# Performance work log

Hardware: AMD Instinct MI355X
Metric: run time of the kernel (lower is better)

## Reference

```python
import jax, jax.numpy as jnp
import numpy as np

E = 256   # hidden_dim
H = 2     # num_heads
DH = E // H
EPS = 1e-5


def setup_inputs() -> dict:
    key = jax.random.key(0)
    ks = jax.random.split(key, 20)
    L, S, MAXLOOP = 8192, 8192, 16
    rel = jax.random.randint(ks[0], (L, MAXLOOP), 0, S)
    # sprinkle some padding sentinels (-1 / -2) like real edge loops
    pad = jax.random.uniform(ks[1], (L, MAXLOOP)) < 0.25
    rel = jnp.where(pad, -1, rel)
    rel = rel.at[:, 0].set(jnp.abs(rel[:, 0]) % S)  # ensure >=1 valid edge per face
    inp = {
        'v_face_edge_loop': rel.astype(jnp.int64) if jax.config.jax_enable_x64 else rel.astype(jnp.int32),
        'v_face_mask': jnp.ones((L,), dtype=bool),
        'v_edge_embedding': jax.random.normal(ks[2], (S, E), jnp.float32),
        'v_face_embedding': jax.random.normal(ks[3], (L, E), jnp.float32),
    }
    def w(k, shape):
        return (jax.random.normal(k, shape, jnp.float32) * 0.02)
    for i, base in ((1, 4), (2, 10)):
        inp[f'w_in{i}'] = w(ks[base + 0], (3 * E, E))
        inp[f'b_in{i}'] = jnp.zeros((3 * E,), jnp.float32)
        inp[f'w_out{i}'] = w(ks[base + 1], (E, E))
        inp[f'b_out{i}'] = jnp.zeros((E,), jnp.float32)
        inp[f'ln{i}_g'] = jnp.ones((E,), jnp.float32)
        inp[f'ln{i}_b'] = jnp.zeros((E,), jnp.float32)
    return inp


def _build_mask(face_edge_loop, S):
    # True = disallowed (torch bool attn_mask semantics).
    L = face_edge_loop.shape[0]
    rel = face_edge_loop
    invalid = (rel == -1) | (rel == -2)
    rel = jnp.where(invalid, S, rel)  # scatter invalids into sentinel column S
    mask = jnp.ones((L, S + 1), dtype=bool)
    mask = mask.at[jnp.arange(L)[:, None], rel].set(False)
    return mask[:, :S]  # [L, S]


def _mha(x, kv, mask, w_in, b_in, w_out, b_out):
    # torch nn.MultiheadAttention (unbatched, eval/no-dropout)
    wq, wk, wv = jnp.split(w_in, 3, axis=0)
    bq, bk, bv = jnp.split(b_in, 3, axis=0)
    L, S = x.shape[0], kv.shape[0]
    q = (x @ wq.T + bq).reshape(L, H, DH)
    k = (kv @ wk.T + bk).reshape(S, H, DH)
    v = (kv @ wv.T + bv).reshape(S, H, DH)
    scores = jnp.einsum('lhd,shd->hls', q, k) / np.sqrt(DH).astype(np.float32)
    scores = jnp.where(mask[None, :, :], jnp.float32(-1e9), scores)
    attn = jax.nn.softmax(scores, axis=-1)          # [H, L, S]
    out = jnp.einsum('hls,shd->lhd', attn, v).reshape(L, E)
    return out @ w_out.T + b_out


def _layernorm(x, g, b):
    m = x.mean(-1, keepdims=True)
    var = ((x - m) ** 2).mean(-1, keepdims=True)
    return (x - m) / jnp.sqrt(var + EPS) * g + b


def reference(v_face_edge_loop, v_face_mask, v_edge_embedding, v_face_embedding,
              w_in1, b_in1, w_out1, b_out1, ln1_g, ln1_b,
              w_in2, b_in2, w_out2, b_out2, ln2_g, ln2_b):
    S = v_edge_embedding.shape[0]
    # v_face_mask is all-True here (static shapes); loop[mask] == loop
    mask = _build_mask(v_face_edge_loop, S)
    x = v_face_embedding
    x = x + _mha(x, v_edge_embedding, mask, w_in1, b_in1, w_out1, b_out1)
    x = _layernorm(x, ln1_g, ln1_b)
    x = x + _mha(x, v_edge_embedding, mask, w_in2, b_in2, w_out2, b_out2)
    x = _layernorm(x, ln2_g, ln2_b)
    return x
```

## Files before the change

kernel.cpp:

```cpp
#include <hip/hip_runtime.h>
#include <hip/hip_bf16.h>

typedef short short8 __attribute__((ext_vector_type(8)));
typedef short short4v __attribute__((ext_vector_type(4)));
typedef float f32x4 __attribute__((ext_vector_type(4)));

#define E 256
#define DH 128

__device__ __forceinline__ float bf2f(__hip_bfloat16 x) { return __bfloat162float(x); }
__device__ __forceinline__ __hip_bfloat16 f2bf(float x) { return __float2bfloat16(x); }

struct CvtArgs { const float* in[6]; __hip_bfloat16* out[6]; int n[6]; };

__global__ __launch_bounds__(256) void f2b_all(CvtArgs a)
{
    int seg = blockIdx.y;
    int i = (blockIdx.x * 256 + threadIdx.x) * 8;
    if (i >= a.n[seg]) return;
    const float* in = a.in[seg];
    float4 x = *reinterpret_cast<const float4*>(in + i);
    float4 y = *reinterpret_cast<const float4*>(in + i + 4);
    __hip_bfloat16* o = a.out[seg] + i;
    o[0] = f2bf(x.x); o[1] = f2bf(x.y); o[2] = f2bf(x.z); o[3] = f2bf(x.w);
    o[4] = f2bf(y.x); o[5] = f2bf(y.y); o[6] = f2bf(y.z); o[7] = f2bf(y.w);
}

struct ProjSeg { const __hip_bfloat16* A; const __hip_bfloat16* W; const float* b; __hip_bfloat16* out; };
struct ProjArgs { ProjSeg seg[5]; };

__global__ __launch_bounds__(256) void gemm_proj(ProjArgs args, int M)
{
    int wv = threadIdx.x >> 6, lane = threadIdx.x & 63;
    int m0 = blockIdx.x * 32;
    if (m0 >= M) return;
    ProjSeg sg = args.seg[blockIdx.y];
    int lo = lane & 15, hi = lane >> 4;

    const __hip_bfloat16* arow0 = sg.A + (size_t)(m0 + lo) * E + hi * 8;
    const __hip_bfloat16* arow1 = arow0 + 16 * E;
    const __hip_bfloat16* brow  = sg.W + (size_t)(wv * 64 + lo) * E + hi * 8;

    f32x4 acc[2][4] = {};
#pragma unroll
    for (int k = 0; k < 8; ++k) {
        short8 a0 = *reinterpret_cast<const short8*>(arow0 + k * 32);
        short8 a1 = *reinterpret_cast<const short8*>(arow1 + k * 32);
#pragma unroll
        for (int nt = 0; nt < 4; ++nt) {
            short8 b = *reinterpret_cast<const short8*>(brow + (size_t)nt * 16 * E + k * 32);
            acc[0][nt] = __builtin_amdgcn_mfma_f32_16x16x32_bf16(a0, b, acc[0][nt], 0, 0, 0);
            acc[1][nt] = __builtin_amdgcn_mfma_f32_16x16x32_bf16(a1, b, acc[1][nt], 0, 0, 0);
        }
    }
#pragma unroll
    for (int nt = 0; nt < 4; ++nt) {
        int col = wv * 64 + nt * 16 + lo;
        float bias = sg.b[col];
#pragma unroll
        for (int mt = 0; mt < 2; ++mt)
#pragma unroll
            for (int r = 0; r < 4; ++r) {
                int row = m0 + mt * 16 + hi * 4 + r;
                sg.out[(size_t)row * E + col] = f2bf(acc[mt][nt][r] + bias);
            }
    }
}

__global__ __launch_bounds__(256) void attn_outproj_ln(
    const int* __restrict__ rel, const __hip_bfloat16* __restrict__ q16,
    const __hip_bfloat16* __restrict__ k16, const __hip_bfloat16* __restrict__ v16,
    const __hip_bfloat16* __restrict__ wout, const float* __restrict__ bout,
    const float* __restrict__ resid, const float* __restrict__ lng, const float* __restrict__ lnb,
    float* __restrict__ xres_out, __hip_bfloat16* __restrict__ xbf_out,
    float* __restrict__ final_out, int L, int ML)
{
    __shared__ __align__(16) __hip_bfloat16 atile[16 * 264];
    __shared__ float sm[16 * 260];
    __shared__ float red[256], red2[256];
    __shared__ float mv[16], rs[16];
    __shared__ __align__(16) float lds_w[4][2][16];
    __shared__ int lds_idx[4][16];

    int tid = threadIdx.x, wv = tid >> 6, lane = tid & 63;
    int m0 = blockIdx.x * 16;
    int g = lane >> 2, q = lane & 3;
    const float scale = 0.088388347648318447f;

    for (int it = 0; it < 4; ++it) {
        int r = wv * 4 + it;
        int face = m0 + r;
        const int* rr = rel + (size_t)face * ML;
        int myidx = (g < ML) ? rr[g] : -1;

        bool dup = false;
#pragma unroll
        for (int d = 1; d < 16; ++d) {
            int other = __shfl(myidx, ((g - d) & 15) * 4 + q);
            if (d <= g && other == myidx) dup = true;
        }
        bool myuse = (myidx >= 0) && !dup;
        int safe = myidx < 0 ? 0 : myidx;
        if (q == 0) lds_idx[wv][g] = safe;

        short8 qv[2][4];
#pragma unroll
        for (int h = 0; h < 2; ++h)
#pragma unroll
            for (int t = 0; t < 4; ++t)
                qv[h][t] = *reinterpret_cast<const short8*>(
                    q16 + (size_t)face * E + h * DH + (t * 4 + q) * 8);

#pragma unroll
        for (int h = 0; h < 2; ++h) {
            const __hip_bfloat16* kbase = k16 + (size_t)safe * E + h * DH;
            float part = 0.f;
#pragma unroll
            for (int t = 0; t < 4; ++t) {
                short8 kvv = *reinterpret_cast<const short8*>(kbase + (t * 4 + q) * 8);
                const __hip_bfloat16* qp = (const __hip_bfloat16*)&qv[h][t];
                const __hip_bfloat16* kp = (const __hip_bfloat16*)&kvv;
#pragma unroll
                for (int e2 = 0; e2 < 8; ++e2)
                    part += bf2f(qp[e2]) * bf2f(kp[e2]);
            }
            part += __shfl_xor(part, 1);
            part += __shfl_xor(part, 2);
            float sc = myuse ? part * scale : -1e30f;
            float mx = sc;
#pragma unroll
            for (int off = 4; off < 64; off <<= 1) mx = fmaxf(mx, __shfl_xor(mx, off));
            float e = __expf(sc - mx);
            float den = e;
#pragma unroll
            for (int off = 4; off < 64; off <<= 1) den += __shfl_xor(den, off);
            if (q == 0) lds_w[wv][h][g] = e / den;
        }

        int h = lane >> 5;
        float a0 = 0.f, a1 = 0.f, a2 = 0.f, a3 = 0.f;
#pragma unroll
        for (int j = 0; j < 16; ++j) {
            int ij = lds_idx[wv][j];
            float wj = lds_w[wv][h][j];
            short4v vv = *reinterpret_cast<const short4v*>(v16 + (size_t)ij * E + 4 * lane);
            const __hip_bfloat16* vp = (const __hip_bfloat16*)&vv;
            a0 += wj * bf2f(vp[0]);
            a1 += wj * bf2f(vp[1]);
            a2 += wj * bf2f(vp[2]);
            a3 += wj * bf2f(vp[3]);
        }
        __hip_bfloat16 ob[4] = {f2bf(a0), f2bf(a1), f2bf(a2), f2bf(a3)};
        *reinterpret_cast<short4v*>(atile + r * 264 + 4 * lane) =
            *reinterpret_cast<const short4v*>(ob);
    }
    __syncthreads();

    const __hip_bfloat16* arow = atile + (lane & 15) * 264 + (lane >> 4) * 8;
    short8 af[8];
#pragma unroll
    for (int kk = 0; kk < 8; ++kk)
        af[kk] = *reinterpret_cast<const short8*>(arow + kk * 32);

#pragma unroll
    for (int ntile = 0; ntile < 4; ++ntile) {
        int n0 = (wv * 4 + ntile) * 16;
        const __hip_bfloat16* brow = wout + (size_t)(n0 + (lane & 15)) * E + (lane >> 4) * 8;
        f32x4 acc = {0.f, 0.f, 0.f, 0.f};
#pragma unroll
        for (int kk = 0; kk < 8; ++kk) {
            short8 b = *reinterpret_cast<const short8*>(brow + kk * 32);
            acc = __builtin_amdgcn_mfma_f32_16x16x32_bf16(af[kk], b, acc, 0, 0, 0);
        }
        int col = n0 + (lane & 15);
#pragma unroll
        for (int r = 0; r < 4; ++r)
            sm[((lane >> 4) * 4 + r) * 260 + col] = acc[r];
    }
    __syncthreads();

    int row = tid >> 4, seg = tid & 15;
    int rowg = m0 + row;
    float s = 0.f, s2 = 0.f;
#pragma unroll
    for (int i = 0; i < 16; ++i) {
        int col = seg + i * 16;
        float v = sm[row * 260 + col] + bout[col] + resid[(size_t)rowg * E + col];
        sm[row * 260 + col] = v;
        s += v; s2 += v * v;
    }
    red[tid] = s; red2[tid] = s2;
    __syncthreads();
    if (tid < 16) {
        float ss = 0.f, ss2 = 0.f;
#pragma unroll
        for (int i = 0; i < 16; ++i) { ss += red[tid * 16 + i]; ss2 += red2[tid * 16 + i]; }
        float mean = ss * (1.f / 256.f);
        float var = ss2 * (1.f / 256.f) - mean * mean;
        mv[tid] = mean;
        rs[tid] = rsqrtf(var + 1e-5f);
    }
    __syncthreads();
    float mean = mv[row], rstd = rs[row];
#pragma unroll
    for (int i = 0; i < 16; ++i) {
        int col = seg + i * 16;
        float y = (sm[row * 260 + col] - mean) * rstd * lng[col] + lnb[col];
        if (final_out) {
            final_out[(size_t)rowg * E + col] = y;
        } else {
            xres_out[(size_t)rowg * E + col] = y;
            xbf_out[(size_t)rowg * E + col] = f2bf(y);
        }
    }
}

extern "C" void kernel_launch(void* const* d_in, const int* in_sizes, int n_in,
                              void* d_out, int out_size, void* d_ws, size_t ws_size,
                              hipStream_t stream) {
    const int* rel = (const int*)d_in[0];
    const float* edge = (const float*)d_in[2];
    const float* face = (const float*)d_in[3];
    const float* w_in[2]  = {(const float*)d_in[4],  (const float*)d_in[10]};
    const float* b_in[2]  = {(const float*)d_in[5],  (const float*)d_in[11]};
    const float* w_out[2] = {(const float*)d_in[6],  (const float*)d_in[12]};
    const float* b_out[2] = {(const float*)d_in[7],  (const float*)d_in[13]};
    const float* ln_g[2]  = {(const float*)d_in[8],  (const float*)d_in[14]};
    const float* ln_b[2]  = {(const float*)d_in[9],  (const float*)d_in[15]};

    int S = in_sizes[2] / E;
    int L = in_sizes[3] / E;
    int ML = in_sizes[0] / L;

    char* ws = (char*)d_ws;
    __hip_bfloat16* face16 = (__hip_bfloat16*)ws; ws += (size_t)L * E * 2;
    __hip_bfloat16* edge16 = (__hip_bfloat16*)ws; ws += (size_t)S * E * 2;
    __hip_bfloat16* q16    = (__hip_bfloat16*)ws; ws += (size_t)L * E * 2;
    __hip_bfloat16* k16[2] = {nullptr, nullptr}, *v16[2] = {nullptr, nullptr};
    for (int l = 0; l < 2; ++l) {
        k16[l] = (__hip_bfloat16*)ws; ws += (size_t)S * E * 2;
        v16[l] = (__hip_bfloat16*)ws; ws += (size_t)S * E * 2;
    }
    __hip_bfloat16* xbf = (__hip_bfloat16*)ws;    ws += (size_t)L * E * 2;
    float* xres = (float*)ws;                     ws += (size_t)L * E * 4;
    __hip_bfloat16* win16[2], *wout16[2];
    for (int l = 0; l < 2; ++l) {
        win16[l]  = (__hip_bfloat16*)ws; ws += (size_t)3 * E * E * 2;
        wout16[l] = (__hip_bfloat16*)ws; ws += (size_t)E * E * 2;
    }

    float* outp = (float*)d_out;

    {
        CvtArgs ca;
        ca.in[0] = face;     ca.out[0] = face16;    ca.n[0] = L * E;
        ca.in[1] = edge;     ca.out[1] = edge16;    ca.n[1] = S * E;
        ca.in[2] = w_in[0];  ca.out[2] = win16[0];  ca.n[2] = 3 * E * E;
        ca.in[3] = w_in[1];  ca.out[3] = win16[1];  ca.n[3] = 3 * E * E;
        ca.in[4] = w_out[0]; ca.out[4] = wout16[0]; ca.n[4] = E * E;
        ca.in[5] = w_out[1]; ca.out[5] = wout16[1]; ca.n[5] = E * E;
        int gx = (L * E) / (256 * 8);
        f2b_all<<<dim3(gx, 6), 256, 0, stream>>>(ca);
    }

    {
        ProjArgs pa;
        pa.seg[0] = {face16, win16[0],                     b_in[0],         q16};
        pa.seg[1] = {edge16, win16[0] + (size_t)E * E,     b_in[0] + E,     k16[0]};
        pa.seg[2] = {edge16, win16[0] + (size_t)2 * E * E, b_in[0] + 2 * E, v16[0]};
        pa.seg[3] = {edge16, win16[1] + (size_t)E * E,     b_in[1] + E,     k16[1]};
        pa.seg[4] = {edge16, win16[1] + (size_t)2 * E * E, b_in[1] + 2 * E, v16[1]};
        gemm_proj<<<dim3(L / 32, 5), 256, 0, stream>>>(pa, L);
    }

    attn_outproj_ln<<<L / 16, 256, 0, stream>>>(rel, q16, k16[0], v16[0],
                                                wout16[0], b_out[0], face,
                                                ln_g[0], ln_b[0],
                                                xres, xbf, nullptr, L, ML);

    {
        ProjArgs pa;
        pa.seg[0] = {xbf, win16[1], b_in[1], q16};
        gemm_proj<<<dim3(L / 32, 1), 256, 0, stream>>>(pa, L);
    }

    attn_outproj_ln<<<L / 16, 256, 0, stream>>>(rel, q16, k16[1], v16[1],
                                                wout16[1], b_out[1], xres,
                                                ln_g[1], ln_b[1],
                                                nullptr, nullptr, outp, L, ML);
}
```

Measured before the change: 207.3 us.

## Use 1024-thread blocks with one wave per face row in attention kernel

The fused attention, out-projection and layernorm kernel now runs 16 waves per block, each handling one face instead of looping over four. Each wave computes one 16-column MFMA tile of the out-projection instead of four, and layernorm becomes a per-wave shuffle reduction with float4 loads and stores, which removes two block barriers and the LDS reduction arrays. The aim is more memory-level parallelism for the gathered K/V loads and less serial looping per wave. The cost is larger blocks with a tighter register budget under the 1024-thread launch bound.

```diff
diff --git a/kernel.cpp b/kernel.cpp
--- a/kernel.cpp
+++ b/kernel.cpp
@@ -67,7 +67,7 @@
     }
 }
 
-__global__ __launch_bounds__(256) void attn_outproj_ln(
+__global__ __launch_bounds__(1024) void attn_outproj_ln(
     const int* __restrict__ rel, const __hip_bfloat16* __restrict__ q16,
     const __hip_bfloat16* __restrict__ k16, const __hip_bfloat16* __restrict__ v16,
     const __hip_bfloat16* __restrict__ wout, const float* __restrict__ bout,
@@ -76,67 +76,58 @@
     float* __restrict__ final_out, int L, int ML)
 {
     __shared__ __align__(16) __hip_bfloat16 atile[16 * 264];
-    __shared__ float sm[16 * 260];
-    __shared__ float red[256], red2[256];
-    __shared__ float mv[16], rs[16];
-    __shared__ __align__(16) float lds_w[4][2][16];
-    __shared__ int lds_idx[4][16];
+    __shared__ __align__(16) float sm[16 * 260];
+    __shared__ __align__(16) float lds_w[16][2][16];
+    __shared__ int lds_idx[16][16];
 
     int tid = threadIdx.x, wv = tid >> 6, lane = tid & 63;
     int m0 = blockIdx.x * 16;
     int g = lane >> 2, q = lane & 3;
+    int face = m0 + wv;
     const float scale = 0.088388347648318447f;
 
-    for (int it = 0; it < 4; ++it) {
-        int r = wv * 4 + it;
-        int face = m0 + r;
-        const int* rr = rel + (size_t)face * ML;
-        int myidx = (g < ML) ? rr[g] : -1;
-
-        bool dup = false;
-#pragma unroll
-        for (int d = 1; d < 16; ++d) {
-            int other = __shfl(myidx, ((g - d) & 15) * 4 + q);
-            if (d <= g && other == myidx) dup = true;
-        }
-        bool myuse = (myidx >= 0) && !dup;
-        int safe = myidx < 0 ? 0 : myidx;
-        if (q == 0) lds_idx[wv][g] = safe;
-
-        short8 qv[2][4];
-#pragma unroll
-        for (int h = 0; h < 2; ++h)
-#pragma unroll
-            for (int t = 0; t < 4; ++t)
-                qv[h][t] = *reinterpret_cast<const short8*>(
-                    q16 + (size_t)face * E + h * DH + (t * 4 + q) * 8);
-
-#pragma unroll
-        for (int h = 0; h < 2; ++h) {
-            const __hip_bfloat16* kbase = k16 + (size_t)safe * E + h * DH;
-            float part = 0.f;
-#pragma unroll
-            for (int t = 0; t < 4; ++t) {
-                short8 kvv = *reinterpret_cast<const short8*>(kbase + (t * 4 + q) * 8);
-                const __hip_bfloat16* qp = (const __hip_bfloat16*)&qv[h][t];
-                const __hip_bfloat16* kp = (const __hip_bfloat16*)&kvv;
-#pragma unroll
-                for (int e2 = 0; e2 < 8; ++e2)
-                    part += bf2f(qp[e2]) * bf2f(kp[e2]);
-            }
-            part += __shfl_xor(part, 1);
-            part += __shfl_xor(part, 2);
-            float sc = myuse ? part * scale : -1e30f;
-            float mx = sc;
-#pragma unroll
-            for (int off = 4; off < 64; off <<= 1) mx = fmaxf(mx, __shfl_xor(mx, off));
-            float e = __expf(sc - mx);
-            float den = e;
-#pragma unroll
-            for (int off = 4; off < 64; off <<= 1) den += __shfl_xor(den, off);
-            if (q == 0) lds_w[wv][h][g] = e / den;
-        }
-
+    const int* rr = rel + (size_t)face * ML;
+    int myidx = (g < ML) ? rr[g] : -1;
+
+    bool dup = false;
+#pragma unroll
+    for (int d = 1; d < 16; ++d) {
+        int other = __shfl(myidx, ((g - d) & 15) * 4 + q);
+        if (d <= g && other == myidx) dup = true;
+    }
+    bool myuse = (myidx >= 0) && !dup;
+    int safe = myidx < 0 ? 0 : myidx;
+    if (q == 0) lds_idx[wv][g] = safe;
+
+#pragma unroll
+    for (int h = 0; h < 2; ++h) {
+        const __hip_bfloat16* kbase = k16 + (size_t)safe * E + h * DH;
+        const __hip_bfloat16* qbase = q16 + (size_t)face * E + h * DH;
+        float part = 0.f;
+#pragma unroll
+        for (int t = 0; t < 4; ++t) {
+            short8 qv = *reinterpret_cast<const short8*>(qbase + (t * 4 + q) * 8);
+            short8 kv = *reinterpret_cast<const short8*>(kbase + (t * 4 + q) * 8);
+            const __hip_bfloat16* qp = (const __hip_bfloat16*)&qv;
+            const __hip_bfloat16* kp = (const __hip_bfloat16*)&kv;
+#pragma unroll
+            for (int e2 = 0; e2 < 8; ++e2)
+                part += bf2f(qp[e2]) * bf2f(kp[e2]);
+        }
+        part += __shfl_xor(part, 1);
+        part += __shfl_xor(part, 2);
+        float sc = myuse ? part * scale : -1e30f;
+        float mx = sc;
+#pragma unroll
+        for (int off = 4; off < 64; off <<= 1) mx = fmaxf(mx, __shfl_xor(mx, off));
+        float e = __expf(sc - mx);
+        float den = e;
+#pragma unroll
+        for (int off = 4; off < 64; off <<= 1) den += __shfl_xor(den, off);
+        if (q == 0) lds_w[wv][h][g] = e / den;
+    }
+
+    {
         int h = lane >> 5;
         float a0 = 0.f, a1 = 0.f, a2 = 0.f, a3 = 0.f;
 #pragma unroll
@@ -151,66 +142,63 @@
             a3 += wj * bf2f(vp[3]);
         }
         __hip_bfloat16 ob[4] = {f2bf(a0), f2bf(a1), f2bf(a2), f2bf(a3)};
-        *reinterpret_cast<short4v*>(atile + r * 264 + 4 * lane) =
+        *reinterpret_cast<short4v*>(atile + wv * 264 + 4 * lane) =
             *reinterpret_cast<const short4v*>(ob);
     }
     __syncthreads();
 
-    const __hip_bfloat16* arow = atile + (lane & 15) * 264 + (lane >> 4) * 8;
-    short8 af[8];
-#pragma unroll
-    for (int kk = 0; kk < 8; ++kk)
-        af[kk] = *reinterpret_cast<const short8*>(arow + kk * 32);
-
-#pragma unroll
-    for (int ntile = 0; ntile < 4; ++ntile) {
-        int n0 = (wv * 4 + ntile) * 16;
-        const __hip_bfloat16* brow = wout + (size_t)(n0 + (lane & 15)) * E + (lane >> 4) * 8;
+    {
+        int lo = lane & 15, hi = lane >> 4;
+        const __hip_bfloat16* arow = atile + lo * 264 + hi * 8;
+        const __hip_bfloat16* brow = wout + (size_t)(wv * 16 + lo) * E + hi * 8;
         f32x4 acc = {0.f, 0.f, 0.f, 0.f};
 #pragma unroll
         for (int kk = 0; kk < 8; ++kk) {
+            short8 a = *reinterpret_cast<const short8*>(arow + kk * 32);
             short8 b = *reinterpret_cast<const short8*>(brow + kk * 32);
-            acc = __builtin_amdgcn_mfma_f32_16x16x32_bf16(af[kk], b, acc, 0, 0, 0);
-        }
-        int col = n0 + (lane & 15);
+            acc = __builtin_amdgcn_mfma_f32_16x16x32_bf16(a, b, acc, 0, 0, 0);
+        }
+        int col = wv * 16 + lo;
 #pragma unroll
         for (int r = 0; r < 4; ++r)
-            sm[((lane >> 4) * 4 + r) * 260 + col] = acc[r];
+            sm[(hi * 4 + r) * 260 + col] = acc[r];
     }
     __syncthreads();
 
-    int row = tid >> 4, seg = tid & 15;
-    int rowg = m0 + row;
-    float s = 0.f, s2 = 0.f;
-#pragma unroll
-    for (int i = 0; i < 16; ++i) {
-        int col = seg + i * 16;
-        float v = sm[row * 260 + col] + bout[col] + resid[(size_t)rowg * E + col];
-        sm[row * 260 + col] = v;
-        s += v; s2 += v * v;
-    }
-    red[tid] = s; red2[tid] = s2;
-    __syncthreads();
-    if (tid < 16) {
-        float ss = 0.f, ss2 = 0.f;
-#pragma unroll
-        for (int i = 0; i < 16; ++i) { ss += red[tid * 16 + i]; ss2 += red2[tid * 16 + i]; }
-        float mean = ss * (1.f / 256.f);
-        float var = ss2 * (1.f / 256.f) - mean * mean;
-        mv[tid] = mean;
-        rs[tid] = rsqrtf(var + 1e-5f);
-    }
-    __syncthreads();
-    float mean = mv[row], rstd = rs[row];
-#pragma unroll
-    for (int i = 0; i < 16; ++i) {
-        int col = seg + i * 16;
-        float y = (sm[row * 260 + col] - mean) * rstd * lng[col] + lnb[col];
+    {
+        int rowg = m0 + wv;
+        float4 pv = *reinterpret_cast<const float4*>(sm + wv * 260 + 4 * lane);
+        float4 rv = *reinterpret_cast<const float4*>(resid + (size_t)rowg * E + 4 * lane);
+        float4 bb = *reinterpret_cast<const float4*>(bout + 4 * lane);
+        float v0 = pv.x + bb.x + rv.x;
+        float v1 = pv.y + bb.y + rv.y;
+        float v2 = pv.z + bb.z + rv.z;
+        float v3 = pv.w + bb.w + rv.w;
+        float s  = v0 + v1 + v2 + v3;
+        float s2 = v0 * v0 + v1 * v1 + v2 * v2 + v3 * v3;
+#pragma unroll
+        for (int off = 1; off < 64; off <<= 1) {
+            s  += __shfl_xor(s, off);
+            s2 += __shfl_xor(s2, off);
+        }
+        float mean = s * (1.f / 256.f);
+        float var  = s2 * (1.f / 256.f) - mean * mean;
+        float rstd = rsqrtf(var + 1e-5f);
+        float4 gg = *reinterpret_cast<const float4*>(lng + 4 * lane);
+        float4 b2 = *reinterpret_cast<const float4*>(lnb + 4 * lane);
+        float y0 = (v0 - mean) * rstd * gg.x + b2.x;
+        float y1 = (v1 - mean) * rstd * gg.y + b2.y;
+        float y2 = (v2 - mean) * rstd * gg.z + b2.z;
+        float y3 = (v3 - mean) * rstd * gg.w + b2.w;
         if (final_out) {
-            final_out[(size_t)rowg * E + col] = y;
+            float4 o = {y0, y1, y2, y3};
+            *reinterpret_cast<float4*>(final_out + (size_t)rowg * E + 4 * lane) = o;
         } else {
-            xres_out[(size_t)rowg * E + col] = y;
-            xbf_out[(size_t)rowg * E + col] = f2bf(y);
+            float4 o = {y0, y1, y2, y3};
+            *reinterpret_cast<float4*>(xres_out + (size_t)rowg * E + 4 * lane) = o;
+            __hip_bfloat16 ob[4] = {f2bf(y0), f2bf(y1), f2bf(y2), f2bf(y3)};
+            *reinterpret_cast<short4v*>(xbf_out + (size_t)rowg * E + 4 * lane) =
+                *reinterpret_cast<const short4v*>(ob);
         }
     }
 }
@@ -236,7 +224,7 @@
     __hip_bfloat16* face16 = (__hip_bfloat16*)ws; ws += (size_t)L * E * 2;
     __hip_bfloat16* edge16 = (__hip_bfloat16*)ws; ws += (size_t)S * E * 2;
     __hip_bfloat16* q16    = (__hip_bfloat16*)ws; ws += (size_t)L * E * 2;
-    __hip_bfloat16* k16[2] = {nullptr, nullptr}, *v16[2] = {nullptr, nullptr};
+    __hip_bfloat16* k16[2], *v16[2];
     for (int l = 0; l < 2; ++l) {
         k16[l] = (__hip_bfloat16*)ws; ws += (size_t)S * E * 2;
         v16[l] = (__hip_bfloat16*)ws; ws += (size_t)S * E * 2;
@@ -273,10 +261,10 @@
         gemm_proj<<<dim3(L / 32, 5), 256, 0, stream>>>(pa, L);
     }
 
-    attn_outproj_ln<<<L / 16, 256, 0, stream>>>(rel, q16, k16[0], v16[0],
-                                                wout16[0], b_out[0], face,
-                                                ln_g[0], ln_b[0],
-                                                xres, xbf, nullptr, L, ML);
+    attn_outproj_ln<<<L / 16, 1024, 0, stream>>>(rel, q16, k16[0], v16[0],
+                                                 wout16[0], b_out[0], face,
+                                                 ln_g[0], ln_b[0],
+                                                 xres, xbf, nullptr, L, ML);
 
     {
         ProjArgs pa;
@@ -284,8 +272,8 @@
         gemm_proj<<<dim3(L / 32, 1), 256, 0, stream>>>(pa, L);
     }
 
-    attn_outproj_ln<<<L / 16, 256, 0, stream>>>(rel, q16, k16[1], v16[1],
-                                                wout16[1], b_out[1], xres,
-                                                ln_g[1], ln_b[1],
-                                                nullptr, nullptr, outp, L, ML);
-}
+    attn_outproj_ln<<<L / 16, 1024, 0, stream>>>(rel, q16, k16[1], v16[1],
+                                                 wout16[1], b_out[1], xres,
+                                                 ln_g[1], ln_b[1],
+                                                 nullptr, nullptr, outp, L, ML);
+}
```

New measurement: 182.8 us. -11.8%, faster.
